# Optimization experiments

Hardware: AMD Instinct MI355X
Metric: run time of the kernel (lower is better)

## Reference

```python
import jax, jax.numpy as jnp
import numpy as np

D_MODEL = 1024
NUM_HEADS = 16


def setup_inputs() -> dict:
    key = jax.random.key(0)
    ks = jax.random.split(key, 5)
    std = np.sqrt(2.0 / (D_MODEL + D_MODEL)).astype(np.float32)
    x = jax.random.normal(ks[0], (4, 2048, D_MODEL), dtype=jnp.float32)
    WQ = jax.random.normal(ks[1], (D_MODEL, D_MODEL), dtype=jnp.float32) * std
    WK = jax.random.normal(ks[2], (D_MODEL, D_MODEL), dtype=jnp.float32) * std
    WV = jax.random.normal(ks[3], (D_MODEL, D_MODEL), dtype=jnp.float32) * std
    WO = jax.random.normal(ks[4], (D_MODEL, D_MODEL), dtype=jnp.float32) * std
    return {"x": x, "WQ": WQ, "WK": WK, "WV": WV, "WO": WO}


def reference(x, WQ, WK, WV, WO):
    B, S, E = x.shape
    H = NUM_HEADS
    dk = E // H
    # project and split heads: [B, H, S, dk]
    def heads(W):
        return jnp.einsum('bse,ef->bsf', x, W).reshape(B, S, H, dk).transpose(0, 2, 1, 3)
    Q, K, V = heads(WQ), heads(WK), heads(WV)
    score = jnp.einsum('bhsd,bhtd->bhst', Q, K) / jnp.sqrt(jnp.float32(dk))
    causal = jnp.tril(jnp.ones((S, S), dtype=bool))  # [S, S]
    score = jnp.where(causal, score, -jnp.inf)
    probs = jax.nn.softmax(score, axis=-1)
    out = jnp.einsum('bhst,bhtd->bhsd', probs, V)  # [B, H, S, dk]
    out = out.transpose(0, 2, 1, 3).reshape(B, S, E)
    return jnp.einsum('bse,ef->bsf', out, WO)
```

## Files before the change

kernel.cpp:

```cpp
#include <hip/hip_runtime.h>

typedef unsigned short u16;
typedef short bf16x8 __attribute__((ext_vector_type(8)));
typedef float f32x4 __attribute__((ext_vector_type(4)));

#define SEQ   2048
#define EMB   1024
#define NH    16
#define DK    64

#define QSCALE 0.1803368801111144f

__device__ __forceinline__ u16 bf16_rne(float f) {
  union { float f; unsigned u; } x;
  x.f = f;
  unsigned u = x.u;
  u += 0x7fffu + ((u >> 16) & 1u);
  return (u16)(u >> 16);
}

__device__ __forceinline__ unsigned cvt_pk_bf16(float a, float b) {
  unsigned r;
  asm("v_cvt_pk_bf16_f32 %0, %1, %2" : "=v"(r) : "v"(a), "v"(b));
  return r;
}

__device__ __forceinline__ float exp2_raw(float x) {
#if __has_builtin(__builtin_amdgcn_exp2f)
  return __builtin_amdgcn_exp2f(x);
#else
  float r; asm("v_exp_f32 %0, %1" : "=v"(r) : "v"(x)); return r;
#endif
}

__device__ __forceinline__ bf16x8 pfrag(unsigned x0, unsigned y0,
                                        unsigned x1, unsigned y1) {
  asm("v_permlane32_swap_b32 %0, %1" : "+v"(x0), "+v"(x1));
  asm("v_permlane32_swap_b32 %0, %1" : "+v"(y0), "+v"(y1));
  asm("v_permlane16_swap_b32 %0, %1" : "+v"(x0), "+v"(x1));
  asm("v_permlane16_swap_b32 %0, %1" : "+v"(y0), "+v"(y1));
  union { unsigned u[4]; bf16x8 v; } f;
  f.u[0] = x0; f.u[1] = y0; f.u[2] = x1; f.u[3] = y1;
  return f.v;
}

#define GLD(src, dst)                                                         \
  __builtin_amdgcn_global_load_lds(                                           \
      (const __attribute__((address_space(1))) void*)(src),                   \
      (__attribute__((address_space(3))) void*)(dst), 16, 0, 0)

__global__ __launch_bounds__(256) void fill_sig(float* __restrict__ out, int n) {
  const int i = blockIdx.x * 256 + threadIdx.x;
  if (i < n) out[i] = 1.0f;
}

__global__ __launch_bounds__(256) void cvt_x(const float* __restrict__ x,
                                             u16* __restrict__ xb) {
  const size_t i = ((size_t)blockIdx.x * 256 + threadIdx.x) * 8;
  float4 v0 = *(const float4*)(x + i);
  float4 v1 = *(const float4*)(x + i + 4);
  union { int4 v; u16 h[8]; } c;
  c.h[0] = bf16_rne(v0.x); c.h[1] = bf16_rne(v0.y);
  c.h[2] = bf16_rne(v0.z); c.h[3] = bf16_rne(v0.w);
  c.h[4] = bf16_rne(v1.x); c.h[5] = bf16_rne(v1.y);
  c.h[6] = bf16_rne(v1.z); c.h[7] = bf16_rne(v1.w);
  *(int4*)(xb + i) = c.v;
}

__global__ __launch_bounds__(256) void tcvt3(
    const float* __restrict__ s0, const float* __restrict__ s1, const float* __restrict__ s2,
    u16* __restrict__ d0, u16* __restrict__ d1, u16* __restrict__ d2) {
  const int z = blockIdx.z;
  const float* src = (z == 0) ? s0 : (z == 1) ? s1 : s2;
  u16* dst = (z == 0) ? d0 : (z == 1) ? d1 : d2;
  const float sc = (z == 0) ? QSCALE : 1.0f;
  __shared__ u16 tile[64][65];
  const int bx = blockIdx.x * 64, by = blockIdx.y * 64;
  for (int i = threadIdx.x; i < 64 * 64; i += 256) {
    const int r = i >> 6, c = i & 63;
    tile[c][r] = bf16_rne(src[(size_t)(by + r) * EMB + bx + c] * sc);
  }
  __syncthreads();
  for (int i = threadIdx.x; i < 64 * 64; i += 256) {
    const int r = i >> 6, c = i & 63;
    dst[(size_t)(bx + r) * EMB + by + c] = tile[r][c];
  }
}

__global__ __launch_bounds__(256) void tcvt1(const float* __restrict__ src,
                                             u16* __restrict__ dst) {
  __shared__ u16 tile[64][65];
  const int bx = blockIdx.x * 64, by = blockIdx.y * 64;
  for (int i = threadIdx.x; i < 64 * 64; i += 256) {
    const int r = i >> 6, c = i & 63;
    tile[c][r] = bf16_rne(src[(size_t)(by + r) * EMB + bx + c]);
  }
  __syncthreads();
  for (int i = threadIdx.x; i < 64 * 64; i += 256) {
    const int r = i >> 6, c = i & 63;
    dst[(size_t)(bx + r) * EMB + by + c] = tile[r][c];
  }
}

__global__ __launch_bounds__(256) void gemm_qkv(
    const u16* __restrict__ A,
    const u16* __restrict__ T0, const u16* __restrict__ T1, const u16* __restrict__ T2,
    u16* __restrict__ C0, u16* __restrict__ C1, u16* __restrict__ C2)
{
  const int z = blockIdx.z;
  const u16* Wt = (z == 0) ? T0 : (z == 1) ? T1 : T2;
  u16* C = (z == 0) ? C0 : (z == 1) ? C1 : C2;

  __shared__ __align__(16) u16 sh[8704];
  u16* const As = sh;
  u16* const Bs = sh + 4096;

  const int tid  = threadIdx.x;
  const int lane = tid & 63;
  const int w    = tid >> 6;
  const int wm   = (w >> 1) * 64;
  const int wn   = (w & 1) * 64;
  const int m0   = blockIdx.x * 128;
  const int n0   = blockIdx.y * 128;

  const int l15  = lane & 15;
  const int g    = lane >> 4;
  const int swz  = (g ^ ((l15 >> 1) & 3)) * 8;

  const int lrow = lane >> 2;
  const int lcol = ((lane & 3) ^ ((lrow >> 1) & 3)) * 8;

  f32x4 acc[4][4] = {};

  for (int k0 = 0; k0 < 1024; k0 += 32) {
#pragma unroll
    for (int i = 0; i < 2; ++i) {
      const int r = w * 32 + i * 16;
      const u16* ga = A  + (size_t)(m0 + r + lrow) * 1024 + (k0 + lcol);
      const u16* gb = Wt + (size_t)(n0 + r + lrow) * 1024 + (k0 + lcol);
      GLD(ga, As + r * 32);
      GLD(gb, Bs + r * 32);
    }
    __syncthreads();
    bf16x8 a[4], b[4];
#pragma unroll
    for (int mi = 0; mi < 4; ++mi)
      a[mi] = *(const bf16x8*)(As + (wm + mi * 16 + l15) * 32 + swz);
#pragma unroll
    for (int ni = 0; ni < 4; ++ni)
      b[ni] = *(const bf16x8*)(Bs + (wn + ni * 16 + l15) * 32 + swz);
#pragma unroll
    for (int mi = 0; mi < 4; ++mi)
#pragma unroll
      for (int ni = 0; ni < 4; ++ni)
        acc[mi][ni] = __builtin_amdgcn_mfma_f32_16x16x32_bf16(a[mi], b[ni], acc[mi][ni], 0, 0, 0);
    __syncthreads();
  }

  const int rb = (lane >> 4) * 4;

  if (z != 2) {
#pragma unroll
    for (int mi = 0; mi < 4; ++mi) {
#pragma unroll
      for (int r = 0; r < 4; ++r) {
        const int row = m0 + wm + mi * 16 + rb + r;
        const int bb = row >> 11, s = row & 2047;
#pragma unroll
        for (int ni = 0; ni < 4; ++ni) {
          const int col = n0 + wn + ni * 16 + l15;
          const int hh = col >> 6, d = col & 63;
          C[((size_t)(bb * NH + hh) * SEQ + s) * DK + d] = bf16_rne(acc[mi][ni][r]);
        }
      }
    }
  } else {
    const int bb = m0 >> 11;
    const int s0 = m0 & 2047;
    u16* const T = sh;
    const int dRd  = tid >> 2;
    const int cbRd = (tid & 3) * 32;
    const int swzR = ((dRd >> 3) & 7) << 3;
#pragma unroll
    for (int p = 0; p < 2; ++p) {
      if ((w & 1) == p) {
#pragma unroll
        for (int mi = 0; mi < 4; ++mi)
#pragma unroll
          for (int r = 0; r < 4; ++r) {
            const int s_local = wm + mi * 16 + rb + r;
#pragma unroll
            for (int ni = 0; ni < 4; ++ni) {
              const int d = ni * 16 + l15;
              T[d * 136 + (s_local ^ (((d >> 3) & 7) << 3))] = bf16_rne(acc[mi][ni][r]);
            }
          }
      }
      __syncthreads();
      u16* dst = C + ((size_t)(bb * NH + (n0 >> 6) + p) * DK + dRd) * SEQ + s0 + cbRd;
#pragma unroll
      for (int k = 0; k < 4; ++k) {
        int4 v = *(const int4*)(T + dRd * 136 + ((cbRd + 8 * k) ^ swzR));
        *(int4*)(dst + 8 * k) = v;
      }
      __syncthreads();
    }
  }
}

__global__ __launch_bounds__(256) void gemm_out(
    const u16* __restrict__ A, const u16* __restrict__ Wt, float* __restrict__ C)
{
  __shared__ __align__(16) u16 As[128 * 32];
  __shared__ __align__(16) u16 Bs[128 * 32];

  const int tid  = threadIdx.x;
  const int lane = tid & 63;
  const int w    = tid >> 6;
  const int wm   = (w >> 1) * 64;
  const int wn   = (w & 1) * 64;
  const int m0   = blockIdx.x * 128;
  const int n0   = blockIdx.y * 128;

  const int l15  = lane & 15;
  const int g    = lane >> 4;
  const int swz  = (g ^ ((l15 >> 1) & 3)) * 8;

  const int lrow = lane >> 2;
  const int lcol = ((lane & 3) ^ ((lrow >> 1) & 3)) * 8;

  f32x4 acc[4][4] = {};

  for (int k0 = 0; k0 < 1024; k0 += 32) {
#pragma unroll
    for (int i = 0; i < 2; ++i) {
      const int r = w * 32 + i * 16;
      const u16* ga = A  + (size_t)(m0 + r + lrow) * 1024 + (k0 + lcol);
      const u16* gb = Wt + (size_t)(n0 + r + lrow) * 1024 + (k0 + lcol);
      GLD(ga, As + r * 32);
      GLD(gb, Bs + r * 32);
    }
    __syncthreads();
    bf16x8 a[4], b[4];
#pragma unroll
    for (int mi = 0; mi < 4; ++mi)
      a[mi] = *(const bf16x8*)(As + (wm + mi * 16 + l15) * 32 + swz);
#pragma unroll
    for (int ni = 0; ni < 4; ++ni)
      b[ni] = *(const bf16x8*)(Bs + (wn + ni * 16 + l15) * 32 + swz);
#pragma unroll
    for (int mi = 0; mi < 4; ++mi)
#pragma unroll
      for (int ni = 0; ni < 4; ++ni)
        acc[mi][ni] = __builtin_amdgcn_mfma_f32_16x16x32_bf16(a[mi], b[ni], acc[mi][ni], 0, 0, 0);
    __syncthreads();
  }

  const int rb = (lane >> 4) * 4;
#pragma unroll
  for (int mi = 0; mi < 4; ++mi) {
#pragma unroll
    for (int r = 0; r < 4; ++r) {
      const int row = m0 + wm + mi * 16 + rb + r;
#pragma unroll
      for (int ni = 0; ni < 4; ++ni) {
        const int col = n0 + wn + ni * 16 + l15;
        C[(size_t)row * 1024 + col] = acc[mi][ni][r];
      }
    }
  }
}

__global__ __launch_bounds__(256) void attn64(
    const u16* __restrict__ Q, const u16* __restrict__ K, const u16* __restrict__ VT,
    u16* __restrict__ O)
{
  const int b   = blockIdx.x;
  const int xcd = b & 7;
  const int bh  = xcd * 8 + ((b >> 3) & 7);
  const int it  = b >> 6;

  const int tid  = threadIdx.x;
  const int lane = tid & 63;
  const int w    = tid >> 6;

  const u16* Qp = Q  + (size_t)bh * SEQ * DK;
  const u16* Kp = K  + (size_t)bh * SEQ * DK;
  const u16* Vp = VT + (size_t)bh * DK * SEQ;

  __shared__ __align__(16) u16 Ks[2][64 * 64];
  __shared__ __align__(16) u16 Vs[2][64 * 64];

  const int l15 = lane & 15;
  const int g   = lane >> 4;
  const int g8  = g * 8;

  const int r_  = tid >> 3;
  const int cS_ = ((tid & 7) ^ (r_ & 7)) * 8;
  const u16* kgA = Kp + (size_t)r_ * DK + cS_;
  const u16* kgB = Kp + (size_t)(r_ + 32) * DK + cS_;
  const u16* vgA = Vp + (size_t)r_ * SEQ + cS_;
  const u16* vgB = Vp + (size_t)(r_ + 32) * SEQ + cS_;

  const int sS0 = ( g      ^ (l15 & 7)) * 8;
  const int sS1 = ((4 + g) ^ (l15 & 7)) * 8;

  const int b_ = bh >> 4, h_ = bh & 15;

  bf16x8 vone;
#pragma unroll
  for (int i = 0; i < 8; ++i) vone[i] = (short)0x3F80;

  for (int pass = 0; pass < 2; ++pass) {
    const int qt = pass ? 15 - it : it;
    const int qw = qt * 128 + w * 32;
    const int tlast = 2 * qt + 1;

    bf16x8 qf[2][2];
#pragma unroll
    for (int j = 0; j < 2; ++j)
#pragma unroll
      for (int kk = 0; kk < 2; ++kk)
        qf[j][kk] = *(const bf16x8*)(Qp + (size_t)(qw + j * 16 + l15) * DK + kk * 32 + g8);

    f32x4 o[2][4] = {};
    f32x4 osum[2] = {};

    GLD(kgA, &Ks[0][0] + tid * 8);
    GLD(kgB, &Ks[0][2048] + tid * 8);
    GLD(vgA, &Vs[0][0] + tid * 8);
    GLD(vgB, &Vs[0][2048] + tid * 8);

    for (int t = 0; t <= tlast; ++t) {
      __syncthreads();
      const int cb = t & 1;
      if (t < tlast) {
        const int nb = cb ^ 1;
        const size_t ko = (size_t)(t + 1) * 64 * DK;
        const int    vo = (t + 1) * 64;
        GLD(kgA + ko, &Ks[nb][0] + tid * 8);
        GLD(kgB + ko, &Ks[nb][2048] + tid * 8);
        GLD(vgA + vo, &Vs[nb][0] + tid * 8);
        GLD(vgB + vo, &Vs[nb][2048] + tid * 8);
      }

      if (64 * t >= qw + 32) continue;

      const u16* const ksb = &Ks[cb][0];
      const u16* const vsb = &Vs[cb][0];

      f32x4 st[2][4] = {};
#pragma unroll
      for (int kk = 0; kk < 2; ++kk) {
        const int so = kk ? sS1 : sS0;
#pragma unroll
        for (int mt = 0; mt < 4; ++mt) {
          const bf16x8 kf = *(const bf16x8*)(ksb + (mt * 16 + l15) * 64 + so);
          st[0][mt] = __builtin_amdgcn_mfma_f32_16x16x32_bf16(kf, qf[0][kk], st[0][mt], 0, 0, 0);
          st[1][mt] = __builtin_amdgcn_mfma_f32_16x16x32_bf16(kf, qf[1][kk], st[1][mt], 0, 0, 0);
        }
      }

      bf16x8 pa[2][2];
#pragma unroll
      for (int j = 0; j < 2; ++j) {
        const int qg = qw + j * 16;
        if (qg <= 64 * t + 48) {
          const int qrow = qg + l15;
#pragma unroll
          for (int mt = 0; mt < 4; ++mt)
#pragma unroll
            for (int r = 0; r < 4; ++r)
              if (64 * t + mt * 16 + g * 4 + r > qrow) st[j][mt][r] = -1e30f;
        }

        unsigned pkx[4], pky[4];
#pragma unroll
        for (int mt = 0; mt < 4; ++mt) {
          float p0 = exp2_raw(st[j][mt][0]);
          float p1 = exp2_raw(st[j][mt][1]);
          float p2 = exp2_raw(st[j][mt][2]);
          float p3 = exp2_raw(st[j][mt][3]);
          pkx[mt] = cvt_pk_bf16(p0, p1);
          pky[mt] = cvt_pk_bf16(p2, p3);
        }
        pa[j][0] = pfrag(pkx[0], pky[0], pkx[1], pky[1]);
        pa[j][1] = pfrag(pkx[2], pky[2], pkx[3], pky[3]);
      }

#pragma unroll
      for (int kk = 0; kk < 2; ++kk) {
        const int so = kk ? sS1 : sS0;
        osum[0] = __builtin_amdgcn_mfma_f32_16x16x32_bf16(pa[0][kk], vone, osum[0], 0, 0, 0);
        osum[1] = __builtin_amdgcn_mfma_f32_16x16x32_bf16(pa[1][kk], vone, osum[1], 0, 0, 0);
#pragma unroll
        for (int nt = 0; nt < 4; ++nt) {
          const bf16x8 vv = *(const bf16x8*)(vsb + (nt * 16 + l15) * 64 + so);
          o[0][nt] = __builtin_amdgcn_mfma_f32_16x16x32_bf16(pa[0][kk], vv, o[0][nt], 0, 0, 0);
          o[1][nt] = __builtin_amdgcn_mfma_f32_16x16x32_bf16(pa[1][kk], vv, o[1][nt], 0, 0, 0);
        }
      }
    }

#pragma unroll
    for (int j = 0; j < 2; ++j) {
#pragma unroll
      for (int r = 0; r < 4; ++r) {
        const float inv = 1.0f / osum[j][r];
        const int   s   = qw + j * 16 + g * 4 + r;
#pragma unroll
        for (int nt = 0; nt < 4; ++nt) {
          const int d = nt * 16 + l15;
          O[((size_t)b_ * SEQ + s) * EMB + h_ * DK + d] = bf16_rne(o[j][nt][r] * inv);
        }
      }
    }
  }
}

extern "C" void kernel_launch(void* const* d_in, const int* in_sizes, int n_in,
                              void* d_out, int out_size, void* d_ws, size_t ws_size,
                              hipStream_t stream) {
  (void)in_sizes; (void)n_in;
  const float* x  = (const float*)d_in[0];
  const float* WQ = (const float*)d_in[1];
  const float* WK = (const float*)d_in[2];
  const float* WV = (const float*)d_in[3];
  const float* WO = (const float*)d_in[4];
  float* out = (float*)d_out;

  const size_t MTOK = (size_t)4 * SEQ;
  const size_t NTOK = MTOK * EMB;
  const size_t NW   = (size_t)EMB * EMB;

  const size_t NEEDED = 4 * NTOK * sizeof(u16);
  if (ws_size < NEEDED) {
    fill_sig<<<dim3((out_size + 255) / 256), 256, 0, stream>>>(out, out_size);
    return;
  }

  u16* ws  = (u16*)d_ws;
  u16* Qb  = ws;
  u16* Kb  = Qb + NTOK;
  u16* VTb = Kb + NTOK;
  u16* Ob  = VTb + NTOK;
  u16* xb  = (u16*)d_out;
  u16* WQt = Ob;
  u16* WKt = WQt + NW;
  u16* WVt = WKt + NW;
  u16* WOt = Qb;

  cvt_x<<<dim3(4096), 256, 0, stream>>>(x, xb);
  tcvt3<<<dim3(16, 16, 3), 256, 0, stream>>>(WQ, WK, WV, WQt, WKt, WVt);
  gemm_qkv<<<dim3(MTOK / 128, EMB / 128, 3), 256, 0, stream>>>(
      xb, WQt, WKt, WVt, Qb, Kb, VTb);
  attn64<<<dim3(512), 256, 0, stream>>>(Qb, Kb, VTb, Ob);
  tcvt1<<<dim3(16, 16), 256, 0, stream>>>(WO, WOt);
  gemm_out<<<dim3(MTOK / 128, EMB / 128), 256, 0, stream>>>(Ob, WOt, out);
}
```

Before: 265.7 us.

## Double-buffer shared-memory tiles in QKV and output projection GEMMs

Both projection GEMM kernels now use two LDS buffers: the next K-slice is loaded into the alternate buffer while MFMAs run on the current one. This drops one of the two barriers per iteration and is meant to hide global-to-LDS load latency behind compute. It doubles shared memory per block to 32KB, which may reduce occupancy. An extra barrier is added before the V transpose epilogue that reuses the shared buffer.

```diff
diff --git a/kernel.cpp b/kernel.cpp
--- a/kernel.cpp
+++ b/kernel.cpp
@@ -111,9 +111,7 @@
   const u16* Wt = (z == 0) ? T0 : (z == 1) ? T1 : T2;
   u16* C = (z == 0) ? C0 : (z == 1) ? C1 : C2;
 
-  __shared__ __align__(16) u16 sh[8704];
-  u16* const As = sh;
-  u16* const Bs = sh + 4096;
+  __shared__ __align__(16) u16 sh[16384];
 
   const int tid  = threadIdx.x;
   const int lane = tid & 63;
@@ -130,18 +128,33 @@
   const int lrow = lane >> 2;
   const int lcol = ((lane & 3) ^ ((lrow >> 1) & 3)) * 8;
 
+  const int r0 = w * 32;
+  const u16* const gaB = A  + (size_t)(m0 + lrow) * 1024 + lcol;
+  const u16* const gbB = Wt + (size_t)(n0 + lrow) * 1024 + lcol;
+
   f32x4 acc[4][4] = {};
 
+#pragma unroll
+  for (int i = 0; i < 2; ++i) {
+    const int r = r0 + i * 16;
+    GLD(gaB + (size_t)r * 1024, sh + r * 32);
+    GLD(gbB + (size_t)r * 1024, sh + 4096 + r * 32);
+  }
+
   for (int k0 = 0; k0 < 1024; k0 += 32) {
-#pragma unroll
-    for (int i = 0; i < 2; ++i) {
-      const int r = w * 32 + i * 16;
-      const u16* ga = A  + (size_t)(m0 + r + lrow) * 1024 + (k0 + lcol);
-      const u16* gb = Wt + (size_t)(n0 + r + lrow) * 1024 + (k0 + lcol);
-      GLD(ga, As + r * 32);
-      GLD(gb, Bs + r * 32);
-    }
     __syncthreads();
+    const int co = ((k0 >> 5) & 1) * 8192;
+    if (k0 + 32 < 1024) {
+      const int no = co ^ 8192;
+#pragma unroll
+      for (int i = 0; i < 2; ++i) {
+        const int r = r0 + i * 16;
+        GLD(gaB + (size_t)r * 1024 + (k0 + 32), sh + no + r * 32);
+        GLD(gbB + (size_t)r * 1024 + (k0 + 32), sh + no + 4096 + r * 32);
+      }
+    }
+    const u16* const As = sh + co;
+    const u16* const Bs = sh + co + 4096;
     bf16x8 a[4], b[4];
 #pragma unroll
     for (int mi = 0; mi < 4; ++mi)
@@ -154,7 +167,6 @@
 #pragma unroll
       for (int ni = 0; ni < 4; ++ni)
         acc[mi][ni] = __builtin_amdgcn_mfma_f32_16x16x32_bf16(a[mi], b[ni], acc[mi][ni], 0, 0, 0);
-    __syncthreads();
   }
 
   const int rb = (lane >> 4) * 4;
@@ -175,6 +187,7 @@
       }
     }
   } else {
+    __syncthreads();
     const int bb = m0 >> 11;
     const int s0 = m0 & 2047;
     u16* const T = sh;
@@ -211,8 +224,7 @@
 __global__ __launch_bounds__(256) void gemm_out(
     const u16* __restrict__ A, const u16* __restrict__ Wt, float* __restrict__ C)
 {
-  __shared__ __align__(16) u16 As[128 * 32];
-  __shared__ __align__(16) u16 Bs[128 * 32];
+  __shared__ __align__(16) u16 sh[16384];
 
   const int tid  = threadIdx.x;
   const int lane = tid & 63;
@@ -229,18 +241,33 @@
   const int lrow = lane >> 2;
   const int lcol = ((lane & 3) ^ ((lrow >> 1) & 3)) * 8;
 
+  const int r0 = w * 32;
+  const u16* const gaB = A  + (size_t)(m0 + lrow) * 1024 + lcol;
+  const u16* const gbB = Wt + (size_t)(n0 + lrow) * 1024 + lcol;
+
   f32x4 acc[4][4] = {};
 
+#pragma unroll
+  for (int i = 0; i < 2; ++i) {
+    const int r = r0 + i * 16;
+    GLD(gaB + (size_t)r * 1024, sh + r * 32);
+    GLD(gbB + (size_t)r * 1024, sh + 4096 + r * 32);
+  }
+
   for (int k0 = 0; k0 < 1024; k0 += 32) {
-#pragma unroll
-    for (int i = 0; i < 2; ++i) {
-      const int r = w * 32 + i * 16;
-      const u16* ga = A  + (size_t)(m0 + r + lrow) * 1024 + (k0 + lcol);
-      const u16* gb = Wt + (size_t)(n0 + r + lrow) * 1024 + (k0 + lcol);
-      GLD(ga, As + r * 32);
-      GLD(gb, Bs + r * 32);
-    }
     __syncthreads();
+    const int co = ((k0 >> 5) & 1) * 8192;
+    if (k0 + 32 < 1024) {
+      const int no = co ^ 8192;
+#pragma unroll
+      for (int i = 0; i < 2; ++i) {
+        const int r = r0 + i * 16;
+        GLD(gaB + (size_t)r * 1024 + (k0 + 32), sh + no + r * 32);
+        GLD(gbB + (size_t)r * 1024 + (k0 + 32), sh + no + 4096 + r * 32);
+      }
+    }
+    const u16* const As = sh + co;
+    const u16* const Bs = sh + co + 4096;
     bf16x8 a[4], b[4];
 #pragma unroll
     for (int mi = 0; mi < 4; ++mi)
@@ -253,7 +280,6 @@
 #pragma unroll
       for (int ni = 0; ni < 4; ++ni)
         acc[mi][ni] = __builtin_amdgcn_mfma_f32_16x16x32_bf16(a[mi], b[ni], acc[mi][ni], 0, 0, 0);
-    __syncthreads();
   }
 
   const int rb = (lane >> 4) * 4;
```

After: 272.4 us. 1.03x slower.
